# Optimization experiments

Hardware: AMD Instinct MI355X
Metric: run time of the kernel (lower is better)

Reference implementation:

```python
import jax, jax.numpy as jnp
import numpy as np

B, N2, N3, D = 16, 1024, 2048, 128


def setup_inputs() -> dict:
    key = jax.random.key(0)
    k1, k2 = jax.random.split(key)
    desc2d = jax.random.normal(k1, (B * N2, D), dtype=jnp.float32)
    desc3d = jax.random.normal(k2, (B * N3, D), dtype=jnp.float32)
    # uniform, sorted batch ids (equal-size segments -> jit-friendly ragged layout)
    idx2d = jnp.repeat(jnp.arange(B, dtype=jnp.int64), N2)
    idx3d = jnp.repeat(jnp.arange(B, dtype=jnp.int64), N3)
    return {"desc2d": desc2d, "idx2d": idx2d, "desc3d": desc3d, "idx3d": idx3d}


def reference(desc2d, idx2d, desc3d, idx3d):
    # number of batches from sorted batch ids (static, computed on host)
    nb = int(np.asarray(idx2d)[-1]) + 1
    n2 = desc2d.shape[0] // nb
    n3 = desc3d.shape[0] // nb
    d2 = desc2d.reshape(nb, n2, -1)  # [B, n2, D]
    d3 = desc3d.reshape(nb, n3, -1)  # [B, n3, D]
    d2 = d2 / jnp.linalg.norm(d2, axis=-1, keepdims=True)
    d3 = d3 / jnp.linalg.norm(d3, axis=-1, keepdims=True)
    sim = jnp.einsum('bid,bjd->bij', d3, d2)  # cosine similarity [B, n3, n2]
    # zero-pad one extra row and column per batch (dustbin), as in the original
    return jnp.pad(sim, ((0, 0), (0, 1), (0, 1)))
```

## Files before the change

kernel.cpp:

```cpp
#include <hip/hip_runtime.h>
#include <hip/hip_bf16.h>

#define NB   16
#define N2   1024
#define N3   2048
#define DD   128
#define OROWS (N3 + 1)
#define OCOLS (N2 + 1)

typedef __attribute__((ext_vector_type(8))) __bf16 bf16x8;
typedef __attribute__((ext_vector_type(4))) float  f32x4;

static __device__ __forceinline__ unsigned short f32_to_bf16(float f) {
    unsigned u = __float_as_uint(f);
    unsigned r = u + 0x7FFF + ((u >> 16) & 1);
    return (unsigned short)(r >> 16);
}

__global__ void normalize_kernel(const float* __restrict__ d2,
                                 const float* __restrict__ d3,
                                 unsigned short* __restrict__ ws) {
    const int row = blockIdx.x * 8 + (threadIdx.x >> 5);
    const int l   = threadIdx.x & 31;
    const float* src = (row < NB * N2)
        ? d2 + (size_t)row * DD
        : d3 + (size_t)(row - NB * N2) * DD;
    const float4 v = *reinterpret_cast<const float4*>(src + l * 4);
    float ss = v.x * v.x + v.y * v.y + v.z * v.z + v.w * v.w;
    #pragma unroll
    for (int off = 16; off; off >>= 1) ss += __shfl_xor(ss, off);
    const float s = rsqrtf(ss);
    ushort4 o;
    o.x = f32_to_bf16(v.x * s);
    o.y = f32_to_bf16(v.y * s);
    o.z = f32_to_bf16(v.z * s);
    o.w = f32_to_bf16(v.w * s);
    *reinterpret_cast<ushort4*>(ws + (size_t)row * DD + l * 4) = o;
}

__global__ __launch_bounds__(512, 1)
void gemm_kernel(const unsigned short* __restrict__ d3n,
                 const unsigned short* __restrict__ d2n,
                 float* __restrict__ out) {
    __shared__ __align__(16) char smem[65536];

    const int hw  = blockIdx.x;
    const int blk = (hw & 7) * 32 + (hw >> 3);
    const int b   = blk >> 4;
    const int ti  = blk & 15;

    const int t = threadIdx.x;

    const char* gA = (const char*)d3n + ((size_t)(b * N3 + ti * 128) << 8);
    const char* gB = (const char*)d2n + ((size_t)(b * N2) << 8);

    #pragma unroll
    for (int it = 0; it < 4; ++it) {
        int o    = it * 8192 + t * 16;
        int row  = o >> 8;
        int scol = (o & 255) ^ ((row & 7) << 4);
        __builtin_amdgcn_global_load_lds(
            (const __attribute__((address_space(1))) void*)(gA + row * 256 + scol),
            (__attribute__((address_space(3))) void*)(smem + o), 16, 0, 0);
    }
    #pragma unroll
    for (int it = 0; it < 2; ++it) {
        int o    = it * 8192 + t * 16;
        int row  = o >> 8;
        int scol = (o & 255) ^ ((row & 7) << 4);
        __builtin_amdgcn_global_load_lds(
            (const __attribute__((address_space(1))) void*)(gB + row * 256 + scol),
            (__attribute__((address_space(3))) void*)(smem + 32768 + o), 16, 0, 0);
    }
    asm volatile("s_waitcnt vmcnt(0)" ::: "memory");
    __builtin_amdgcn_s_barrier();
    __builtin_amdgcn_sched_barrier(0);

    const int wid = t >> 6;
    const int l   = t & 63;
    const int wm  = (wid >> 2) * 64;
    const int wn  = (wid & 3) * 16;
    const int lr  = l & 15;
    const int kq  = l >> 4;
    const int sw  = (lr & 7) << 4;

    bf16x8 af[4][4];
    #pragma unroll
    for (int ks = 0; ks < 4; ++ks) {
        const int kb = ks * 64 + kq * 16;
        #pragma unroll
        for (int mi = 0; mi < 4; ++mi) {
            int r = wm + mi * 16 + lr;
            af[ks][mi] = *reinterpret_cast<const bf16x8*>(smem + r * 256 + (kb ^ sw));
        }
    }

    float* obase = out + (size_t)b * OROWS * OCOLS + (size_t)(ti * 128) * OCOLS;

    for (int nj = 0; nj < 16; ++nj) {
        const char* bbuf = smem + 32768 + (nj & 1) * 16384;

        f32x4 acc[4] = {};
        #pragma unroll
        for (int ks = 0; ks < 4; ++ks) {
            const int kb = ks * 64 + kq * 16;
            int r = wn + lr;
            bf16x8 bfr = *reinterpret_cast<const bf16x8*>(bbuf + r * 256 + (kb ^ sw));
            #pragma unroll
            for (int mi = 0; mi < 4; ++mi)
                acc[mi] = __builtin_amdgcn_mfma_f32_16x16x32_bf16(
                    af[ks][mi], bfr, acc[mi], 0, 0, 0);
        }

        if (nj < 15) {
            const char* gBn = gB + (size_t)(nj + 1) * 16384;
            char* nbuf = smem + 32768 + ((nj + 1) & 1) * 16384;
            #pragma unroll
            for (int it = 0; it < 2; ++it) {
                int o    = it * 8192 + t * 16;
                int row  = o >> 8;
                int scol = (o & 255) ^ ((row & 7) << 4);
                __builtin_amdgcn_global_load_lds(
                    (const __attribute__((address_space(1))) void*)(gBn + row * 256 + scol),
                    (__attribute__((address_space(3))) void*)(smem + ((nbuf - smem) + o)), 16, 0, 0);
            }
        }

        #pragma unroll
        for (int mi = 0; mi < 4; ++mi) {
            #pragma unroll
            for (int i = 0; i < 4; ++i) {
                int r = wm + mi * 16 + kq * 4 + i;
                int c = nj * 64 + wn + lr;
                obase[(size_t)r * OCOLS + c] = acc[mi][i];
            }
        }

        asm volatile("s_waitcnt vmcnt(16)" ::: "memory");
        __builtin_amdgcn_s_barrier();
        __builtin_amdgcn_sched_barrier(0);
    }

    if (t < 128)
        obase[(size_t)t * OCOLS + N2] = 0.0f;
    if (ti == 15) {
        float* last = out + (size_t)b * OROWS * OCOLS + (size_t)N3 * OCOLS;
        for (int c = t; c < OCOLS; c += 512) last[c] = 0.0f;
    }
}

extern "C" void kernel_launch(void* const* d_in, const int* in_sizes, int n_in,
                              void* d_out, int out_size, void* d_ws, size_t ws_size,
                              hipStream_t stream) {
    (void)in_sizes; (void)n_in; (void)out_size; (void)ws_size;
    const float* desc2d = (const float*)d_in[0];
    const float* desc3d = (const float*)d_in[2];

    unsigned short* d2n = (unsigned short*)d_ws;
    unsigned short* d3n = d2n + (size_t)NB * N2 * DD;
    float* out = (float*)d_out;

    normalize_kernel<<<(NB * (N2 + N3)) / 8, 256, 0, stream>>>(desc2d, desc3d, d2n);
    gemm_kernel<<<NB * (N3 / 128), 512, 0, stream>>>(d3n, d2n, out);
}
```

Measured before the change: 40.28 us.

## Fuse row normalization into GEMM kernel, loading fp32 and converting in registers

Removes the separate normalize kernel and its bf16 workspace round trip. The GEMM kernel now loads fp32 rows directly, computes norms with lane shuffles, converts to bf16 and writes swizzled tiles into LDS, prefetching the next B tile into registers during the MFMA loop. This saves a kernel launch and workspace traffic. In exchange, each block re-reads and re-normalizes the fp32 B rows of its batch (16 blocks per batch), doubling the bytes per B load. It also replaces async global-to-LDS loads with register staging, which adds VGPR pressure and ALU work inside the loop.

New measurement: 44.03 us. +9.3%, slower.

```diff
diff --git a/kernel.cpp b/kernel.cpp
--- a/kernel.cpp
+++ b/kernel.cpp
@@ -11,37 +11,18 @@
 typedef __attribute__((ext_vector_type(8))) __bf16 bf16x8;
 typedef __attribute__((ext_vector_type(4))) float  f32x4;
 
-static __device__ __forceinline__ unsigned short f32_to_bf16(float f) {
-    unsigned u = __float_as_uint(f);
-    unsigned r = u + 0x7FFF + ((u >> 16) & 1);
-    return (unsigned short)(r >> 16);
-}
-
-__global__ void normalize_kernel(const float* __restrict__ d2,
-                                 const float* __restrict__ d3,
-                                 unsigned short* __restrict__ ws) {
-    const int row = blockIdx.x * 8 + (threadIdx.x >> 5);
-    const int l   = threadIdx.x & 31;
-    const float* src = (row < NB * N2)
-        ? d2 + (size_t)row * DD
-        : d3 + (size_t)(row - NB * N2) * DD;
-    const float4 v = *reinterpret_cast<const float4*>(src + l * 4);
-    float ss = v.x * v.x + v.y * v.y + v.z * v.z + v.w * v.w;
-    #pragma unroll
-    for (int off = 16; off; off >>= 1) ss += __shfl_xor(ss, off);
-    const float s = rsqrtf(ss);
-    ushort4 o;
-    o.x = f32_to_bf16(v.x * s);
-    o.y = f32_to_bf16(v.y * s);
-    o.z = f32_to_bf16(v.z * s);
-    o.w = f32_to_bf16(v.w * s);
-    *reinterpret_cast<ushort4*>(ws + (size_t)row * DD + l * 4) = o;
+static __device__ __forceinline__ unsigned pack_bf16x2(float a, float b) {
+    unsigned ua = __float_as_uint(a);
+    ua = (ua + 0x7FFF + ((ua >> 16) & 1)) >> 16;
+    unsigned ub = __float_as_uint(b);
+    ub = (ub + 0x7FFF + ((ub >> 16) & 1)) & 0xFFFF0000u;
+    return ua | ub;
 }
 
 __global__ __launch_bounds__(512, 1)
-void gemm_kernel(const unsigned short* __restrict__ d3n,
-                 const unsigned short* __restrict__ d2n,
-                 float* __restrict__ out) {
+void fused_kernel(const float* __restrict__ d2,
+                  const float* __restrict__ d3,
+                  float* __restrict__ out) {
     __shared__ __align__(16) char smem[65536];
 
     const int hw  = blockIdx.x;
@@ -51,28 +32,65 @@
 
     const int t = threadIdx.x;
 
-    const char* gA = (const char*)d3n + ((size_t)(b * N3 + ti * 128) << 8);
-    const char* gB = (const char*)d2n + ((size_t)(b * N2) << 8);
+    const float* gA = d3 + ((size_t)(b * N3 + ti * 128)) * DD;
+    const float* gB = d2 + ((size_t)b * N2) * DD;
 
+    const int arow  = t >> 2;
+    const int apart = t & 3;
+    float4 av[8];
     #pragma unroll
-    for (int it = 0; it < 4; ++it) {
-        int o    = it * 8192 + t * 16;
-        int row  = o >> 8;
-        int scol = (o & 255) ^ ((row & 7) << 4);
-        __builtin_amdgcn_global_load_lds(
-            (const __attribute__((address_space(1))) void*)(gA + row * 256 + scol),
-            (__attribute__((address_space(3))) void*)(smem + o), 16, 0, 0);
+    for (int i = 0; i < 8; ++i)
+        av[i] = *reinterpret_cast<const float4*>(gA + (size_t)arow * DD + apart * 32 + i * 4);
+
+    const int brow  = t >> 3;
+    const int bpart = t & 7;
+    float4 bv[4];
+    #pragma unroll
+    for (int i = 0; i < 4; ++i)
+        bv[i] = *reinterpret_cast<const float4*>(gB + (size_t)brow * DD + bpart * 16 + i * 4);
+
+    {
+        float ss = 0.f;
+        #pragma unroll
+        for (int i = 0; i < 8; ++i)
+            ss += av[i].x * av[i].x + av[i].y * av[i].y + av[i].z * av[i].z + av[i].w * av[i].w;
+        ss += __shfl_xor(ss, 1);
+        ss += __shfl_xor(ss, 2);
+        const float s = rsqrtf(ss);
+        const int aswz = (arow & 7) << 4;
+        #pragma unroll
+        for (int j = 0; j < 4; ++j) {
+            uint4 w;
+            w.x = pack_bf16x2(av[2*j].x * s,   av[2*j].y * s);
+            w.y = pack_bf16x2(av[2*j].z * s,   av[2*j].w * s);
+            w.z = pack_bf16x2(av[2*j+1].x * s, av[2*j+1].y * s);
+            w.w = pack_bf16x2(av[2*j+1].z * s, av[2*j+1].w * s);
+            int colb = apart * 64 + j * 16;
+            *reinterpret_cast<uint4*>(smem + arow * 256 + (colb ^ aswz)) = w;
+        }
     }
-    #pragma unroll
-    for (int it = 0; it < 2; ++it) {
-        int o    = it * 8192 + t * 16;
-        int row  = o >> 8;
-        int scol = (o & 255) ^ ((row & 7) << 4);
-        __builtin_amdgcn_global_load_lds(
-            (const __attribute__((address_space(1))) void*)(gB + row * 256 + scol),
-            (__attribute__((address_space(3))) void*)(smem + 32768 + o), 16, 0, 0);
+    {
+        float ss = 0.f;
+        #pragma unroll
+        for (int i = 0; i < 4; ++i)
+            ss += bv[i].x * bv[i].x + bv[i].y * bv[i].y + bv[i].z * bv[i].z + bv[i].w * bv[i].w;
+        ss += __shfl_xor(ss, 1);
+        ss += __shfl_xor(ss, 2);
+        ss += __shfl_xor(ss, 4);
+        const float s = rsqrtf(ss);
+        const int bswz = (brow & 7) << 4;
+        #pragma unroll
+        for (int j = 0; j < 2; ++j) {
+            uint4 w;
+            w.x = pack_bf16x2(bv[2*j].x * s,   bv[2*j].y * s);
+            w.y = pack_bf16x2(bv[2*j].z * s,   bv[2*j].w * s);
+            w.z = pack_bf16x2(bv[2*j+1].x * s, bv[2*j+1].y * s);
+            w.w = pack_bf16x2(bv[2*j+1].z * s, bv[2*j+1].w * s);
+            int colb = bpart * 32 + j * 16;
+            *reinterpret_cast<uint4*>(smem + 32768 + brow * 256 + (colb ^ bswz)) = w;
+        }
     }
-    asm volatile("s_waitcnt vmcnt(0)" ::: "memory");
+    asm volatile("s_waitcnt lgkmcnt(0)" ::: "memory");
     __builtin_amdgcn_s_barrier();
     __builtin_amdgcn_sched_barrier(0);
 
@@ -98,32 +116,23 @@
     float* obase = out + (size_t)b * OROWS * OCOLS + (size_t)(ti * 128) * OCOLS;
 
     for (int nj = 0; nj < 16; ++nj) {
+        if (nj < 15) {
+            const float* gc = gB + (size_t)(nj + 1) * 64 * DD;
+            #pragma unroll
+            for (int i = 0; i < 4; ++i)
+                bv[i] = *reinterpret_cast<const float4*>(gc + (size_t)brow * DD + bpart * 16 + i * 4);
+        }
+
         const char* bbuf = smem + 32768 + (nj & 1) * 16384;
-
         f32x4 acc[4] = {};
         #pragma unroll
         for (int ks = 0; ks < 4; ++ks) {
             const int kb = ks * 64 + kq * 16;
-            int r = wn + lr;
-            bf16x8 bfr = *reinterpret_cast<const bf16x8*>(bbuf + r * 256 + (kb ^ sw));
+            bf16x8 bfr = *reinterpret_cast<const bf16x8*>(bbuf + (wn + lr) * 256 + (kb ^ sw));
             #pragma unroll
             for (int mi = 0; mi < 4; ++mi)
                 acc[mi] = __builtin_amdgcn_mfma_f32_16x16x32_bf16(
                     af[ks][mi], bfr, acc[mi], 0, 0, 0);
-        }
-
-        if (nj < 15) {
-            const char* gBn = gB + (size_t)(nj + 1) * 16384;
-            char* nbuf = smem + 32768 + ((nj + 1) & 1) * 16384;
-            #pragma unroll
-            for (int it = 0; it < 2; ++it) {
-                int o    = it * 8192 + t * 16;
-                int row  = o >> 8;
-                int scol = (o & 255) ^ ((row & 7) << 4);
-                __builtin_amdgcn_global_load_lds(
-                    (const __attribute__((address_space(1))) void*)(gBn + row * 256 + scol),
-                    (__attribute__((address_space(3))) void*)(smem + ((nbuf - smem) + o)), 16, 0, 0);
-            }
         }
 
         #pragma unroll
@@ -136,7 +145,30 @@
             }
         }
 
-        asm volatile("s_waitcnt vmcnt(16)" ::: "memory");
+        if (nj < 15) {
+            float ss = 0.f;
+            #pragma unroll
+            for (int i = 0; i < 4; ++i)
+                ss += bv[i].x * bv[i].x + bv[i].y * bv[i].y + bv[i].z * bv[i].z + bv[i].w * bv[i].w;
+            ss += __shfl_xor(ss, 1);
+            ss += __shfl_xor(ss, 2);
+            ss += __shfl_xor(ss, 4);
+            const float s = rsqrtf(ss);
+            const int bswz = (brow & 7) << 4;
+            char* nb = smem + 32768 + ((nj + 1) & 1) * 16384;
+            #pragma unroll
+            for (int j = 0; j < 2; ++j) {
+                uint4 w;
+                w.x = pack_bf16x2(bv[2*j].x * s,   bv[2*j].y * s);
+                w.y = pack_bf16x2(bv[2*j].z * s,   bv[2*j].w * s);
+                w.z = pack_bf16x2(bv[2*j+1].x * s, bv[2*j+1].y * s);
+                w.w = pack_bf16x2(bv[2*j+1].z * s, bv[2*j+1].w * s);
+                int colb = bpart * 32 + j * 16;
+                *reinterpret_cast<uint4*>(nb + brow * 256 + (colb ^ bswz)) = w;
+            }
+            asm volatile("s_waitcnt lgkmcnt(0)" ::: "memory");
+        }
+        asm volatile("" ::: "memory");
         __builtin_amdgcn_s_barrier();
         __builtin_amdgcn_sched_barrier(0);
     }
@@ -152,14 +184,10 @@
 extern "C" void kernel_launch(void* const* d_in, const int* in_sizes, int n_in,
                               void* d_out, int out_size, void* d_ws, size_t ws_size,
                               hipStream_t stream) {
-    (void)in_sizes; (void)n_in; (void)out_size; (void)ws_size;
+    (void)in_sizes; (void)n_in; (void)out_size; (void)d_ws; (void)ws_size;
     const float* desc2d = (const float*)d_in[0];
     const float* desc3d = (const float*)d_in[2];
-
-    unsigned short* d2n = (unsigned short*)d_ws;
-    unsigned short* d3n = d2n + (size_t)NB * N2 * DD;
     float* out = (float*)d_out;
 
-    normalize_kernel<<<(NB * (N2 + N3)) / 8, 256, 0, stream>>>(desc2d, desc3d, d2n);
-    gemm_kernel<<<NB * (N3 / 128), 512, 0, stream>>>(d3n, d2n, out);
+    fused_kernel<<<NB * (N3 / 128), 512, 0, stream>>>(desc2d, desc3d, out);
 }
```
